# Performance work log

Hardware: AMD Instinct MI355X
Metric: run time of the kernel (lower is better)

The kernel has to match this reference:

```python
import jax, jax.numpy as jnp
import numpy as np


def setup_inputs() -> dict:
    key = jax.random.key(0)
    k1, k2, k3, k4 = jax.random.split(key, 4)
    B, T, C, H = 256, 320, 1024, 64
    x = jax.random.normal(k1, (B, T, C), dtype=jnp.float32)
    # nn.Linear weights stored as (in, out) for x @ W
    scale = 1.0 / np.sqrt(C)
    W_key = jax.random.normal(k2, (C, H), dtype=jnp.float32) * scale
    W_query = jax.random.normal(k3, (C, H), dtype=jnp.float32) * scale
    W_value = jax.random.normal(k4, (C, H), dtype=jnp.float32) * scale
    return {"x": x, "W_key": W_key, "W_query": W_query, "W_value": W_value}


def reference(x, W_key, W_query, W_value):
    # Single-head causal self-attention. Dropout is identity (eval mode).
    B, T, C = x.shape
    k = x @ W_key     # [B,T,H]
    q = x @ W_query   # [B,T,H]
    v = x @ W_value   # [B,T,H]
    # NOTE: source scales by C**-0.5 with C = embd_size (input dim), not head_size.
    scale = jnp.asarray(C, x.dtype) ** -0.5
    wei = jnp.einsum("bth,bsh->bts", q, k) * scale  # [B,T,T]
    causal = jnp.tril(jnp.ones((T, T), dtype=bool))
    wei = jnp.where(causal, wei, -jnp.inf)
    wei = jax.nn.softmax(wei, axis=-1)
    out = jnp.einsum("bts,bsh->bth", wei, v)  # [B,T,H]
    return out
```

## Files before the change

kernel.cpp:

```cpp
#include <hip/hip_runtime.h>

typedef __bf16 bf16;
typedef __bf16 bf16x4 __attribute__((ext_vector_type(4)));
typedef __bf16 bf16x8 __attribute__((ext_vector_type(8)));
typedef float f32x4 __attribute__((ext_vector_type(4)));

#define MFMA16(a, b, c) __builtin_amdgcn_mfma_f32_16x16x32_bf16((a), (b), (c), 0, 0, 0)

#define GLD16(gp, lp)                                                              \
  __builtin_amdgcn_global_load_lds(                                                \
      (const __attribute__((address_space(1))) unsigned int*)(unsigned long long)(gp), \
      (__attribute__((address_space(3))) unsigned int*)(unsigned long long)(lp), 16, 0, 0)


__global__ __launch_bounds__(256) void wtrans_kernel(
    const float* __restrict__ Wk, const float* __restrict__ Wq,
    const float* __restrict__ Wv, bf16* __restrict__ Wt) {
  __shared__ bf16 tile[64][65];
  const int mat = blockIdx.x >> 4;
  const int kt = (blockIdx.x & 15) << 6;
  const float* __restrict__ W = (mat == 0) ? Wk : ((mat == 1) ? Wq : Wv);
  const int tid = threadIdx.x;
#pragma unroll
  for (int j = 0; j < 16; ++j) {
    const int i = tid + 256 * j;
    const int k = i >> 6, h = i & 63;
    tile[h][k] = (bf16)W[(kt + k) * 64 + h];
  }
  __syncthreads();
#pragma unroll
  for (int j = 0; j < 16; ++j) {
    const int i = tid + 256 * j;
    const int h = i >> 6, k = i & 63;
    Wt[mat * 65536 + h * 1024 + kt + k] = tile[h][k];
  }
}

__global__ __launch_bounds__(256) void qkv_kernel(
    const float* __restrict__ x, const bf16* __restrict__ Wt,
    bf16* __restrict__ Qw, bf16* __restrict__ Kw, bf16* __restrict__ Vt) {
  __shared__ __align__(16) bf16 Ws[2][192 * 64];
  const int tid = threadIdx.x;
  const int w = tid >> 6, l = tid & 63;
  const int lr = l & 15, lg = l >> 4;
  const int m0 = blockIdx.x * 64;
  const int r0 = m0 + 16 * w;

  f32x4 acc[12];
#pragma unroll
  for (int nf = 0; nf < 12; ++nf) acc[nf] = (f32x4)0.0f;

  const char* wsrc[6];
#pragma unroll
  for (int j = 0; j < 6; ++j) {
    const int g = 48 * w + 8 * j + (l >> 3);
    wsrc[j] = (const char*)(Wt + (g >> 6) * 65536 + (g & 63) * 1024) +
              (((l & 7) * 16) ^ ((g & 7) << 4));
  }
  auto wdma = [&](int t) {
    char* lb = (char*)&Ws[t & 1][0];
#pragma unroll
    for (int j = 0; j < 6; ++j)
      GLD16(wsrc[j] + t * 128, lb + (48 * w + 8 * j) * 128);
  };

  const char* xsrc = (const char*)(x + (size_t)(r0 + lr) * 1024) + lg * 32;
  f32x4 gA[4], gB[4];
  auto xload = [&](int t, f32x4* g) {
    const char* p = xsrc + t * 256;
    g[0] = *(const f32x4*)(p);
    g[1] = *(const f32x4*)(p + 16);
    g[2] = *(const f32x4*)(p + 128);
    g[3] = *(const f32x4*)(p + 144);
  };

  wdma(0);
  xload(0, gA);
  xload(1, gB);

  const int sw = (lr & 7) << 4;
  auto step = [&](int t, f32x4* g) {
    if (t < 15) {
      asm volatile("s_waitcnt vmcnt(4)" ::: "memory");
    } else {
      asm volatile("s_waitcnt vmcnt(0)" ::: "memory");
    }
    __builtin_amdgcn_sched_barrier(0);
    __builtin_amdgcn_s_barrier();
    __builtin_amdgcn_sched_barrier(0);

    bf16x8 a0, a1;
#pragma unroll
    for (int i = 0; i < 4; ++i) {
      a0[i] = (bf16)g[0][i]; a0[4 + i] = (bf16)g[1][i];
      a1[i] = (bf16)g[2][i]; a1[4 + i] = (bf16)g[3][i];
    }
    if (t < 15) wdma(t + 1);
    if (t < 14) xload(t + 2, g);

    const char* wb = (const char*)&Ws[t & 1][0];
#pragma unroll
    for (int nf = 0; nf < 12; ++nf) {
      const char* rp = wb + (nf * 16 + lr) * 128;
      const bf16x8 b0 = *(const bf16x8*)(rp + ((lg * 16) ^ sw));
      const bf16x8 b1 = *(const bf16x8*)(rp + ((64 + lg * 16) ^ sw));
      acc[nf] = MFMA16(a0, b0, acc[nf]);
      acc[nf] = MFMA16(a1, b1, acc[nf]);
    }
  };

#pragma unroll
  for (int t2 = 0; t2 < 16; t2 += 2) {
    step(t2, gA);
    step(t2 + 1, gB);
  }

#pragma unroll
  for (int nf = 0; nf < 12; ++nf) {
    const int mat = nf >> 2;
    const int h = (nf & 3) * 16 + lr;
    const int mb = r0 + lg * 4;
    if (mat == 2) {
      const int bb = mb / 320, tt = mb % 320;
      bf16x4 o;
#pragma unroll
      for (int r = 0; r < 4; ++r) o[r] = (bf16)acc[nf][r];
      *(bf16x4*)(Vt + ((size_t)bb * 64 + h) * 320 + tt) = o;
    } else {
      bf16* __restrict__ dst = (mat == 0) ? Kw : Qw;
#pragma unroll
      for (int r = 0; r < 4; ++r) dst[(size_t)(mb + r) * 64 + h] = (bf16)acc[nf][r];
    }
  }
}

template <int QT>
__device__ __forceinline__ void attn_impl(
    int b, const bf16* __restrict__ Qw, const bf16* __restrict__ Kw,
    const bf16* __restrict__ Vt, float* __restrict__ out,
    char* Ks, char* Vs, char* Ps) {
  constexpr int NT = QT + 1;
  const int tid = threadIdx.x;
  const int w = tid >> 6, l = tid & 63;
  const int lr = l & 15, lg = l >> 4;
  const int t0 = QT * 64 + w * 16;
  const int tq = t0 + lr;

  const bf16* qp = Qw + ((size_t)b * 320 + tq) * 64 + lg * 8;
  const bf16x8 bq0 = *(const bf16x8*)qp;
  const bf16x8 bq1 = *(const bf16x8*)(qp + 32);

  f32x4 acc[NT * 4];
#pragma unroll
  for (int i = 0; i < NT * 4; ++i) acc[i] = (f32x4)0.0f;

  bf16x8 kg0, kg1;
  const int krow = w * 16 + (l >> 2);
  const int kcb = (l & 3) * 16;
  const int ksw = (krow & 7) << 4;
  auto gloadK = [&](int st) {
    const bf16* src = Kw + ((size_t)b * 320 + st * 64 + krow) * 64 + (l & 3) * 8;
    kg0 = *(const bf16x8*)src;
    kg1 = *(const bf16x8*)(src + 32);
  };
  auto dswriteK = [&](int buf) {
    char* base = Ks + buf * 8192 + krow * 128;
    *(bf16x8*)(base + (kcb ^ ksw)) = kg0;
    *(bf16x8*)(base + ((kcb + 64) ^ ksw)) = kg1;
  };

  gloadK(0);
  dswriteK(0);
  asm volatile("s_waitcnt lgkmcnt(0)" ::: "memory");
  __builtin_amdgcn_s_barrier();

  const int asw = (lr & 7) << 4;
#pragma unroll
  for (int st = 0; st < NT; ++st) {
    if (st < QT) gloadK(st + 1);
    const char* kb = Ks + (st & 1) * 8192;
#pragma unroll
    for (int nf = 0; nf < 4; ++nf) {
      const char* rp = kb + (nf * 16 + lr) * 128;
      const bf16x8 a0 = *(const bf16x8*)(rp + ((lg * 16) ^ asw));
      const bf16x8 a1 = *(const bf16x8*)(rp + ((64 + lg * 16) ^ asw));
      acc[st * 4 + nf] = MFMA16(a0, bq0, acc[st * 4 + nf]);
      acc[st * 4 + nf] = MFMA16(a1, bq1, acc[st * 4 + nf]);
    }
    if (st < QT) {
      dswriteK((st + 1) & 1);
      asm volatile("s_waitcnt lgkmcnt(0)" ::: "memory");
      __builtin_amdgcn_s_barrier();
    }
  }

  uint2 vg[4];
  const int vrow = w * 16 + (l >> 4);
  auto gloadV = [&](int st) {
    const bf16* src = Vt + ((size_t)b * 64 + vrow) * 320 + st * 64 + (l & 15) * 4;
#pragma unroll
    for (int i = 0; i < 4; ++i) vg[i] = *(const uint2*)(src + i * 4 * 320);
  };
  auto dswriteV = [&](int buf) {
#pragma unroll
    for (int i = 0; i < 4; ++i) {
      const int hl = vrow + i * 4;
      *(uint2*)(Vs + buf * 8192 + hl * 128 + (((l & 15) * 8) ^ ((hl & 7) << 4))) = vg[i];
    }
  };
  gloadV(0);

  float mx = -1e30f;
#pragma unroll
  for (int st = 0; st < NT; ++st)
#pragma unroll
    for (int nf = 0; nf < 4; ++nf)
#pragma unroll
      for (int r = 0; r < 4; ++r) {
        const int sg = st * 64 + nf * 16 + lg * 4 + r;
        float v = acc[st * 4 + nf][r] * 0.03125f;
        v = (sg > tq) ? -1e30f : v;
        acc[st * 4 + nf][r] = v;
        mx = fmaxf(mx, v);
      }
  mx = fmaxf(mx, __shfl_xor(mx, 16));
  mx = fmaxf(mx, __shfl_xor(mx, 32));
  float sum = 0.f;
#pragma unroll
  for (int i = 0; i < NT * 4; ++i)
#pragma unroll
    for (int r = 0; r < 4; ++r) {
      const float p = __expf(acc[i][r] - mx);
      acc[i][r] = p;
      sum += p;
    }
  sum += __shfl_xor(sum, 16);
  sum += __shfl_xor(sum, 32);
  const float rinv = 1.0f / sum;

  dswriteV(0);
  asm volatile("s_waitcnt lgkmcnt(0)" ::: "memory");
  __builtin_amdgcn_s_barrier();

  char* Pw = Ps + w * 2048;
  f32x4 ao[4];
#pragma unroll
  for (int hf = 0; hf < 4; ++hf) ao[hf] = (f32x4)0.0f;

#pragma unroll
  for (int st = 0; st < NT; ++st) {
    if (st < QT) gloadV(st + 1);
#pragma unroll
    for (int nf = 0; nf < 4; ++nf) {
      bf16x4 o;
#pragma unroll
      for (int r = 0; r < 4; ++r) o[r] = (bf16)(acc[st * 4 + nf][r] * rinv);
      *(bf16x4*)(Pw + lr * 128 + ((nf * 32 + lg * 8) ^ asw)) = o;
    }
    const char* vb = Vs + (st & 1) * 8192;
#pragma unroll
    for (int ks = 0; ks < 2; ++ks) {
      const bf16x8 ap = *(const bf16x8*)(Pw + lr * 128 + ((ks * 64 + lg * 16) ^ asw));
#pragma unroll
      for (int hf = 0; hf < 4; ++hf) {
        const bf16x8 bv =
            *(const bf16x8*)(vb + (hf * 16 + lr) * 128 + ((ks * 64 + lg * 16) ^ asw));
        ao[hf] = MFMA16(ap, bv, ao[hf]);
      }
    }
    if (st < QT) {
      dswriteV((st + 1) & 1);
      asm volatile("s_waitcnt lgkmcnt(0)" ::: "memory");
      __builtin_amdgcn_s_barrier();
    }
  }

  const int rowb = t0 + lg * 4;
#pragma unroll
  for (int hf = 0; hf < 4; ++hf)
#pragma unroll
    for (int r = 0; r < 4; ++r)
      out[((size_t)b * 320 + rowb + r) * 64 + hf * 16 + lr] = ao[hf][r];
}

__global__ __launch_bounds__(256) void attn_kernel(
    const bf16* __restrict__ Qw, const bf16* __restrict__ Kw,
    const bf16* __restrict__ Vt, float* __restrict__ out) {
  __shared__ __align__(16) char Ks[2 * 8192];
  __shared__ __align__(16) char Vs[2 * 8192];
  __shared__ __align__(16) char Ps[4 * 2048];
  const int b = blockIdx.x;
  const int qt = 4 - blockIdx.y;
  switch (qt) {
    case 0: attn_impl<0>(b, Qw, Kw, Vt, out, Ks, Vs, Ps); break;
    case 1: attn_impl<1>(b, Qw, Kw, Vt, out, Ks, Vs, Ps); break;
    case 2: attn_impl<2>(b, Qw, Kw, Vt, out, Ks, Vs, Ps); break;
    case 3: attn_impl<3>(b, Qw, Kw, Vt, out, Ks, Vs, Ps); break;
    default: attn_impl<4>(b, Qw, Kw, Vt, out, Ks, Vs, Ps); break;
  }
}

extern "C" void kernel_launch(void* const* d_in, const int* in_sizes, int n_in,
                              void* d_out, int out_size, void* d_ws, size_t ws_size,
                              hipStream_t stream) {
  const float* x  = (const float*)d_in[0];
  const float* Wk = (const float*)d_in[1];
  const float* Wq = (const float*)d_in[2];
  const float* Wv = (const float*)d_in[3];
  float* out = (float*)d_out;

  bf16* Wt = (bf16*)d_ws;
  bf16* Qw = Wt + 3 * 64 * 1024;
  bf16* Kw = Qw + (size_t)81920 * 64;
  bf16* Vt = Kw + (size_t)81920 * 64;

  hipLaunchKernelGGL(wtrans_kernel, dim3(48), dim3(256), 0, stream, Wk, Wq, Wv, Wt);
  hipLaunchKernelGGL(qkv_kernel, dim3(1280), dim3(256), 0, stream, x, Wt, Qw, Kw, Vt);
  hipLaunchKernelGGL(attn_kernel, dim3(256, 5), dim3(256), 0, stream, Qw, Kw, Vt, out);
}
```

Baseline: 115.8 us.

## Rewrite QKV projection as single-wave 32x32 MFMA tiles with direct global weight loads

Replaces the 4-wave QKV projection block, which double-buffered the transposed weights in LDS via global_load_lds, with one-wave blocks of 32 rows. Each block loads x and the bf16 weights straight from global memory and uses 32x32x16 MFMAs. Results are staged through LDS so Q/K and the transposed V are written with coalesced vector stores. This drops LDS weight staging and the barriers, but each wave now re-reads the full weight matrix from cache with no explicit prefetch pipelining, and the grid has many more blocks.

After: 279.5 us. 2.41x slower.

```diff
diff --git a/kernel.cpp b/kernel.cpp
--- a/kernel.cpp
+++ b/kernel.cpp
@@ -4,13 +4,10 @@
 typedef __bf16 bf16x4 __attribute__((ext_vector_type(4)));
 typedef __bf16 bf16x8 __attribute__((ext_vector_type(8)));
 typedef float f32x4 __attribute__((ext_vector_type(4)));
+typedef float f32x16 __attribute__((ext_vector_type(16)));
 
 #define MFMA16(a, b, c) __builtin_amdgcn_mfma_f32_16x16x32_bf16((a), (b), (c), 0, 0, 0)
-
-#define GLD16(gp, lp)                                                              \
-  __builtin_amdgcn_global_load_lds(                                                \
-      (const __attribute__((address_space(1))) unsigned int*)(unsigned long long)(gp), \
-      (__attribute__((address_space(3))) unsigned int*)(unsigned long long)(lp), 16, 0, 0)
+#define MFMA32(a, b, c) __builtin_amdgcn_mfma_f32_32x32x16_bf16((a), (b), (c), 0, 0, 0)
 
 
 __global__ __launch_bounds__(256) void wtrans_kernel(
@@ -36,101 +33,73 @@
   }
 }
 
-__global__ __launch_bounds__(256) void qkv_kernel(
+__global__ __launch_bounds__(64) void qkv_kernel(
     const float* __restrict__ x, const bf16* __restrict__ Wt,
     bf16* __restrict__ Qw, bf16* __restrict__ Kw, bf16* __restrict__ Vt) {
-  __shared__ __align__(16) bf16 Ws[2][192 * 64];
-  const int tid = threadIdx.x;
-  const int w = tid >> 6, l = tid & 63;
-  const int lr = l & 15, lg = l >> 4;
-  const int m0 = blockIdx.x * 64;
-  const int r0 = m0 + 16 * w;
-
-  f32x4 acc[12];
-#pragma unroll
-  for (int nf = 0; nf < 12; ++nf) acc[nf] = (f32x4)0.0f;
-
-  const char* wsrc[6];
-#pragma unroll
-  for (int j = 0; j < 6; ++j) {
-    const int g = 48 * w + 8 * j + (l >> 3);
-    wsrc[j] = (const char*)(Wt + (g >> 6) * 65536 + (g & 63) * 1024) +
-              (((l & 7) * 16) ^ ((g & 7) << 4));
-  }
-  auto wdma = [&](int t) {
-    char* lb = (char*)&Ws[t & 1][0];
-#pragma unroll
-    for (int j = 0; j < 6; ++j)
-      GLD16(wsrc[j] + t * 128, lb + (48 * w + 8 * j) * 128);
-  };
-
-  const char* xsrc = (const char*)(x + (size_t)(r0 + lr) * 1024) + lg * 32;
-  f32x4 gA[4], gB[4];
-  auto xload = [&](int t, f32x4* g) {
-    const char* p = xsrc + t * 256;
-    g[0] = *(const f32x4*)(p);
-    g[1] = *(const f32x4*)(p + 16);
-    g[2] = *(const f32x4*)(p + 128);
-    g[3] = *(const f32x4*)(p + 144);
-  };
-
-  wdma(0);
-  xload(0, gA);
-  xload(1, gB);
-
-  const int sw = (lr & 7) << 4;
-  auto step = [&](int t, f32x4* g) {
-    if (t < 15) {
-      asm volatile("s_waitcnt vmcnt(4)" ::: "memory");
-    } else {
-      asm volatile("s_waitcnt vmcnt(0)" ::: "memory");
-    }
-    __builtin_amdgcn_sched_barrier(0);
-    __builtin_amdgcn_s_barrier();
-    __builtin_amdgcn_sched_barrier(0);
-
-    bf16x8 a0, a1;
+  __shared__ __align__(16) bf16 Cs[192 * 40];
+  const int l = threadIdx.x;
+  const int m0 = blockIdx.x * 32;
+  const int row = l & 31, kg = l >> 5;
+
+  f32x16 acc[6];
+#pragma unroll
+  for (int nf = 0; nf < 6; ++nf) acc[nf] = (f32x16)0.0f;
+
+  const float* xp = x + (size_t)(m0 + row) * 1024 + kg * 8;
+  const bf16* wp[6];
+#pragma unroll
+  for (int nf = 0; nf < 6; ++nf)
+    wp[nf] = Wt + (nf >> 1) * 65536 + ((nf & 1) * 32 + row) * 1024 + kg * 8;
+
+#pragma unroll 2
+  for (int ks = 0; ks < 64; ++ks) {
+    const f32x4 xa = *(const f32x4*)(xp);
+    const f32x4 xb = *(const f32x4*)(xp + 4);
+    bf16x8 a;
 #pragma unroll
     for (int i = 0; i < 4; ++i) {
-      a0[i] = (bf16)g[0][i]; a0[4 + i] = (bf16)g[1][i];
-      a1[i] = (bf16)g[2][i]; a1[4 + i] = (bf16)g[3][i];
-    }
-    if (t < 15) wdma(t + 1);
-    if (t < 14) xload(t + 2, g);
-
-    const char* wb = (const char*)&Ws[t & 1][0];
-#pragma unroll
-    for (int nf = 0; nf < 12; ++nf) {
-      const char* rp = wb + (nf * 16 + lr) * 128;
-      const bf16x8 b0 = *(const bf16x8*)(rp + ((lg * 16) ^ sw));
-      const bf16x8 b1 = *(const bf16x8*)(rp + ((64 + lg * 16) ^ sw));
-      acc[nf] = MFMA16(a0, b0, acc[nf]);
-      acc[nf] = MFMA16(a1, b1, acc[nf]);
-    }
-  };
-
-#pragma unroll
-  for (int t2 = 0; t2 < 16; t2 += 2) {
-    step(t2, gA);
-    step(t2 + 1, gB);
-  }
-
-#pragma unroll
-  for (int nf = 0; nf < 12; ++nf) {
-    const int mat = nf >> 2;
-    const int h = (nf & 3) * 16 + lr;
-    const int mb = r0 + lg * 4;
-    if (mat == 2) {
-      const int bb = mb / 320, tt = mb % 320;
+      a[i] = (bf16)xa[i];
+      a[4 + i] = (bf16)xb[i];
+    }
+#pragma unroll
+    for (int nf = 0; nf < 6; ++nf) {
+      const bf16x8 b = *(const bf16x8*)(wp[nf]);
+      acc[nf] = MFMA32(a, b, acc[nf]);
+      wp[nf] += 16;
+    }
+    xp += 16;
+  }
+
+#pragma unroll
+  for (int nf = 0; nf < 6; ++nf)
+#pragma unroll
+    for (int q = 0; q < 4; ++q) {
       bf16x4 o;
 #pragma unroll
-      for (int r = 0; r < 4; ++r) o[r] = (bf16)acc[nf][r];
-      *(bf16x4*)(Vt + ((size_t)bb * 64 + h) * 320 + tt) = o;
-    } else {
-      bf16* __restrict__ dst = (mat == 0) ? Kw : Qw;
-#pragma unroll
-      for (int r = 0; r < 4; ++r) dst[(size_t)(mb + r) * 64 + h] = (bf16)acc[nf][r];
-    }
+      for (int r = 0; r < 4; ++r) o[r] = (bf16)acc[nf][q * 4 + r];
+      *(bf16x4*)(Cs + (nf * 32 + row) * 40 + 8 * q + 4 * kg) = o;
+    }
+
+  const int r = l >> 1, c = l & 1;
+#pragma unroll
+  for (int m = 0; m < 2; ++m) {
+    bf16* __restrict__ dst = ((m == 0) ? Kw : Qw) + (size_t)(m0 + r) * 64 + c * 32;
+    const int cb = m * 64 + c * 32;
+#pragma unroll
+    for (int v = 0; v < 4; ++v) {
+      bf16x8 o;
+#pragma unroll
+      for (int s = 0; s < 8; ++s) o[s] = Cs[(cb + v * 8 + s) * 40 + r];
+      *(bf16x8*)(dst + v * 8) = o;
+    }
+  }
+  {
+    const int bb = m0 / 320, tt0 = m0 % 320;
+    const bf16* src = Cs + (128 + l) * 40;
+    bf16* __restrict__ dst = Vt + ((size_t)bb * 64 + l) * 320 + tt0;
+#pragma unroll
+    for (int v = 0; v < 4; ++v)
+      *(bf16x8*)(dst + v * 8) = *(const bf16x8*)(src + v * 8);
   }
 }
 
@@ -315,6 +284,6 @@
   bf16* Vt = Kw + (size_t)81920 * 64;
 
   hipLaunchKernelGGL(wtrans_kernel, dim3(48), dim3(256), 0, stream, Wk, Wq, Wv, Wt);
-  hipLaunchKernelGGL(qkv_kernel, dim3(1280), dim3(256), 0, stream, x, Wt, Qw, Kw, Vt);
+  hipLaunchKernelGGL(qkv_kernel, dim3(2560), dim3(64), 0, stream, x, Wt, Qw, Kw, Vt);
   hipLaunchKernelGGL(attn_kernel, dim3(256, 5), dim3(256), 0, stream, Qw, Kw, Vt, out);
 }
```
